# Kernel optimization log

Measured on AMD Instinct MI355X. Metric: run time of the kernel, lower is better.

Reference implementation:

```python
import jax, jax.numpy as jnp
import numpy as np

N_NODES = 131072
N_GRAPHS = 4096
D_Z = 512      # backbone_dout
D_X = 256      # node_dim
D_U = 64       # glob_din
D_H = 512      # dhid
D_IN = D_Z + D_X
N_EDGES = 2097152


def setup_inputs() -> dict:
    key = jax.random.key(0)
    ks = jax.random.split(key, 24)
    s = 0.02
    inp = {
        "z": jax.random.normal(ks[0], (N_NODES, D_Z), jnp.float32),
        "u": jax.random.normal(ks[1], (N_GRAPHS, D_U), jnp.float32),
        "x": jax.random.normal(ks[2], (N_NODES, D_X), jnp.float32),
        "prev_h": jax.random.normal(ks[3], (N_NODES, D_H), jnp.float32),
        "edge_index": jax.random.randint(ks[4], (2, N_EDGES), 0, N_NODES, jnp.int64),
        "batch": jnp.sort(jax.random.randint(ks[5], (N_NODES,), 0, N_GRAPHS, jnp.int64)),
        "batch_size": N_GRAPHS,
        # GConvGRU with K=1: each ChebConv is a plain Linear (T_0 term only)
        "Wxz": jax.random.normal(ks[6], (D_IN, D_H), jnp.float32) * s,
        "bxz": jnp.zeros((D_H,), jnp.float32),
        "Whz": jax.random.normal(ks[7], (D_H, D_H), jnp.float32) * s,
        "bhz": jnp.zeros((D_H,), jnp.float32),
        "Wxr": jax.random.normal(ks[8], (D_IN, D_H), jnp.float32) * s,
        "bxr": jnp.zeros((D_H,), jnp.float32),
        "Whr": jax.random.normal(ks[9], (D_H, D_H), jnp.float32) * s,
        "bhr": jnp.zeros((D_H,), jnp.float32),
        "Wxh": jax.random.normal(ks[10], (D_IN, D_H), jnp.float32) * s,
        "bxh": jnp.zeros((D_H,), jnp.float32),
        "Whh": jax.random.normal(ks[11], (D_H, D_H), jnp.float32) * s,
        "bhh": jnp.zeros((D_H,), jnp.float32),
        # GraphAndGlobalFusion.global_proj
        "Wg": jax.random.normal(ks[12], (D_U, D_Z), jnp.float32) * s,
        "bg": jnp.zeros((D_Z,), jnp.float32),
    }
    return inp


def reference(z, u, x, prev_h, Wxz, bxz, Whz, bhz, Wxr, bxr, Whr, bhr,
              Wxh, bxh, Whh, bhh, Wg, bg, edge_index, batch, batch_size):
    # --- GConvGRU (K=1 ChebConv => per-node linear; edge_index unused) ---
    X = jnp.concatenate([z, x], axis=-1)                       # [N, D_IN]
    Z = jax.nn.sigmoid(X @ Wxz + bxz + prev_h @ Whz + bhz)     # update gate
    R = jax.nn.sigmoid(X @ Wxr + bxr + prev_h @ Whr + bhr)     # reset gate
    H_tilde = jnp.tanh(X @ Wxh + bxh + (prev_h * R) @ Whh + bhh)
    H = Z * prev_h + (1.0 - Z) * H_tilde                       # [N, D_H]
    # --- GraphAndGlobalFusion ---
    graph_emb = jax.ops.segment_sum(z, batch, num_segments=batch_size)  # [B, D_Z]
    glob_emb = jax.nn.relu(u @ Wg + bg)                                 # [B, D_Z]
    fused_emb = jnp.concatenate([graph_emb, glob_emb], axis=-1)         # [B, 2*D_Z]
    return fused_emb, H
```

## Files before the change

### kernel.cpp

```cpp
#include <hip/hip_runtime.h>
#include <hip/hip_bf16.h>

#define N_NODES 131072
#define N_GRAPHS 4096
#define D_Z 512
#define D_X 256
#define D_U 64
#define D_H 512
#define D_IN 768
#define KTOT 1280
#define NG1 1024

using bf16   = __bf16;
using bf16x8 = __attribute__((ext_vector_type(8))) __bf16;
using f32x4  = __attribute__((ext_vector_type(4))) float;
using fl4    = __attribute__((ext_vector_type(4))) float;

__device__ __forceinline__ void gload_lds16(const void* g, void* lds) {
    __builtin_amdgcn_global_load_lds(
        (const __attribute__((address_space(1))) unsigned int*)g,
        (__attribute__((address_space(3))) unsigned int*)lds,
        16, 0, 0);
}

__global__ void prep_weights(const float* __restrict__ Wxz, const float* __restrict__ Whz,
                             const float* __restrict__ Wxr, const float* __restrict__ Whr,
                             const float* __restrict__ Wxh, const float* __restrict__ Whh,
                             const float* __restrict__ bxz, const float* __restrict__ bhz,
                             const float* __restrict__ bxr, const float* __restrict__ bhr,
                             const float* __restrict__ bxh, const float* __restrict__ bhh,
                             bf16* __restrict__ WT1, bf16* __restrict__ WT2,
                             float* __restrict__ bias1, float* __restrict__ bias2)
{
    int idx = blockIdx.x * blockDim.x + threadIdx.x;
    if (idx < NG1)
        bias1[idx] = (idx < D_H) ? (bxz[idx] + bhz[idx]) : (bxr[idx - D_H] + bhr[idx - D_H]);
    if (idx < D_H)
        bias2[idx] = bxh[idx] + bhh[idx];

    const int T1 = NG1 * (KTOT / 8);
    if (idx < T1) {
        int n = idx % NG1, kc = idx / NG1, k0 = kc * 8;
        int col = (n < D_H) ? n : n - D_H;
        const float* Wx = (n < D_H) ? Wxz : Wxr;
        const float* Wh = (n < D_H) ? Whz : Whr;
        bf16x8 o;
        #pragma unroll
        for (int i = 0; i < 8; ++i) {
            int k = k0 + i;
            float f = (k < D_IN) ? Wx[(long)k * D_H + col] : Wh[(long)(k - D_IN) * D_H + col];
            o[i] = (bf16)f;
        }
        *(bf16x8*)(WT1 + (long)n * KTOT + k0) = o;
    } else {
        int j = idx - T1;
        int n = j % D_H, kc = j / D_H, k0 = kc * 8;
        bf16x8 o;
        #pragma unroll
        for (int i = 0; i < 8; ++i) {
            int k = k0 + i;
            float f = (k < D_IN) ? Wxh[(long)k * D_H + n] : Whh[(long)(k - D_IN) * D_H + n];
            o[i] = (bf16)f;
        }
        *(bf16x8*)(WT2 + (long)n * KTOT + k0) = o;
    }
}

__global__ void prep_A(const float* __restrict__ z, const float* __restrict__ x,
                       const float* __restrict__ ph, bf16* __restrict__ Abf)
{
    long idx = (long)blockIdx.x * blockDim.x + threadIdx.x;
    long row = idx / 160;
    int  e   = (int)(idx % 160) * 8;
    const float* src;
    if (e < D_Z)        src = z  + row * D_Z + e;
    else if (e < D_IN)  src = x  + row * D_X + (e - D_Z);
    else                src = ph + row * D_H + (e - D_IN);
    fl4 v0 = *(const fl4*)src;
    fl4 v1 = *(const fl4*)(src + 4);
    bf16x8 o;
    o[0]=(bf16)v0[0]; o[1]=(bf16)v0[1]; o[2]=(bf16)v0[2]; o[3]=(bf16)v0[3];
    o[4]=(bf16)v1[0]; o[5]=(bf16)v1[1]; o[6]=(bf16)v1[2]; o[7]=(bf16)v1[3];
    *(bf16x8*)(Abf + row * KTOT + e) = o;
}

template<int NCOLS, int MODE>
__global__ __launch_bounds__(256, 4)
void gemm_kernel(const bf16* __restrict__ A,
                 const bf16* __restrict__ A2,
                 const bf16* __restrict__ W,
                 const float* __restrict__ bias,
                 float* __restrict__ Hout,
                 bf16* __restrict__ Rapp_out)
{
    __shared__ __align__(16) char Atile[16384];
    __shared__ __align__(16) char Btile[16384];

    const int tid = threadIdx.x;
    const int w = tid >> 6, l = tid & 63;

    constexpr int nb  = NCOLS / 128;
    constexpr int nwg = (N_NODES / 128) * nb;
    constexpr int cpx = nwg / 8;
    const int bid = blockIdx.x;
    const int swz = (bid & 7) * cpx + (bid >> 3);
    const int  bn = swz % nb;
    const long m0 = (long)(swz / nb) * 128;
    const int  n0 = bn * 128;

    const int trow = tid >> 3;
    const int tg   = tid & 7;
    const int kes  = ((tg * 16) ^ ((trow & 7) << 4)) >> 1;

    f32x4 acc[4][4];
    #pragma unroll
    for (int i = 0; i < 4; ++i)
        #pragma unroll
        for (int j = 0; j < 4; ++j) acc[i][j] = f32x4{0.f, 0.f, 0.f, 0.f};

    const int wr = w >> 1, wc = w & 1;
    const int lr = l & 15, lg = l >> 4;

    for (int k0 = 0; k0 < KTOT; k0 += 64) {
        __syncthreads();
        const bf16* Asrc; long astr; int kofs;
        if (MODE == 2 && k0 >= D_IN) { Asrc = A2; astr = D_H;  kofs = k0 - D_IN; }
        else                         { Asrc = A;  astr = KTOT; kofs = k0; }
        #pragma unroll
        for (int r = 0; r < 4; ++r)
            gload_lds16(Asrc + (m0 + r * 32 + trow) * astr + kofs + kes,
                        Atile + r * 4096 + tid * 16);
        #pragma unroll
        for (int r = 0; r < 4; ++r)
            gload_lds16(W + (long)(n0 + r * 32 + trow) * KTOT + k0 + kes,
                        Btile + r * 4096 + tid * 16);
        __syncthreads();

        #pragma unroll
        for (int ks = 0; ks < 2; ++ks) {
            bf16x8 af[4];
            #pragma unroll
            for (int mi = 0; mi < 4; ++mi) {
                int row = wr * 64 + mi * 16 + lr;
                int addr = (row << 7) + ((ks * 64 + lg * 16) ^ ((row & 7) << 4));
                af[mi] = *(const bf16x8*)(Atile + addr);
            }
            #pragma unroll
            for (int ni = 0; ni < 4; ++ni) {
                int row = wc * 64 + ni * 16 + lr;
                int addr = (row << 7) + ((ks * 64 + lg * 16) ^ ((row & 7) << 4));
                bf16x8 bfr = *(const bf16x8*)(Btile + addr);
                #pragma unroll
                for (int mi = 0; mi < 4; ++mi)
                    acc[mi][ni] = __builtin_amdgcn_mfma_f32_16x16x32_bf16(
                        af[mi], bfr, acc[mi][ni], 0, 0, 0);
            }
        }
    }

    #pragma unroll
    for (int mi = 0; mi < 4; ++mi) {
        #pragma unroll
        for (int ni = 0; ni < 4; ++ni) {
            int gc = n0 + wc * 64 + ni * 16 + lr;
            float bv = bias[gc];
            #pragma unroll
            for (int j = 0; j < 4; ++j) {
                long gr = m0 + wr * 64 + mi * 16 + lg * 4 + j;
                float v = acc[mi][ni][j] + bv;
                if (MODE == 1) {
                    float s = 1.f / (1.f + __expf(-v));
                    if (NCOLS == NG1 && n0 < D_H) {
                        Hout[gr * D_H + gc] = s;
                    } else {
                        float ph = (float)A[gr * KTOT + D_IN + (gc - D_H)];
                        Rapp_out[gr * D_H + (gc - D_H)] = (bf16)(s * ph);
                    }
                } else {
                    float ht = 2.f / (1.f + __expf(-2.f * v)) - 1.f;
                    long  o  = gr * D_H + gc;
                    float zz = Hout[o];
                    float ph = (float)A[gr * KTOT + D_IN + gc];
                    Hout[o] = zz * ph + (1.f - zz) * ht;
                }
            }
        }
    }
}

__global__ __launch_bounds__(256)
void fusion_kernel(const float* __restrict__ z, const float* __restrict__ u,
                   const float* __restrict__ Wg, const float* __restrict__ bg,
                   const int* __restrict__ batch, float* __restrict__ out)
{
    int g = blockIdx.x;
    __shared__ float us[D_U];
    __shared__ int   rng[2];
    int tid = threadIdx.x;
    if (tid < D_U) us[tid] = u[(long)g * D_U + tid];
    if (tid < 2) {
        int target = g + tid;
        int lo = 0, hi = N_NODES;
        while (lo < hi) { int mid = (lo + hi) >> 1; if (batch[mid] < target) lo = mid + 1; else hi = mid; }
        rng[tid] = lo;
    }
    __syncthreads();
    int start = rng[0], end = rng[1];
    int d0 = tid * 2;
    float s0 = 0.f, s1 = 0.f;
    for (int n = start; n < end; ++n) {
        const float* zp = z + (long)n * D_Z + d0;
        s0 += zp[0]; s1 += zp[1];
    }
    long ob = (long)g * 1024;
    out[ob + d0]     = s0;
    out[ob + d0 + 1] = s1;
    float a0 = bg[d0], a1 = bg[d0 + 1];
    #pragma unroll 8
    for (int k = 0; k < D_U; ++k) {
        float uv = us[k];
        a0 += uv * Wg[k * D_Z + d0];
        a1 += uv * Wg[k * D_Z + d0 + 1];
    }
    out[ob + 512 + d0]     = fmaxf(a0, 0.f);
    out[ob + 512 + d0 + 1] = fmaxf(a1, 0.f);
}

extern "C" void kernel_launch(void* const* d_in, const int* in_sizes, int n_in,
                              void* d_out, int out_size, void* d_ws, size_t ws_size,
                              hipStream_t stream) {
    (void)in_sizes; (void)n_in; (void)out_size; (void)ws_size;
    const float* z      = (const float*)d_in[0];
    const float* u      = (const float*)d_in[1];
    const float* x      = (const float*)d_in[2];
    const float* prev_h = (const float*)d_in[3];
    const int*   batch  = (const int*)d_in[5];
    const float* Wxz = (const float*)d_in[7];
    const float* bxz = (const float*)d_in[8];
    const float* Whz = (const float*)d_in[9];
    const float* bhz = (const float*)d_in[10];
    const float* Wxr = (const float*)d_in[11];
    const float* bxr = (const float*)d_in[12];
    const float* Whr = (const float*)d_in[13];
    const float* bhr = (const float*)d_in[14];
    const float* Wxh = (const float*)d_in[15];
    const float* bxh = (const float*)d_in[16];
    const float* Whh = (const float*)d_in[17];
    const float* bhh = (const float*)d_in[18];
    const float* Wg  = (const float*)d_in[19];
    const float* bg  = (const float*)d_in[20];

    char* ws = (char*)d_ws;
    bf16*  WT1   = (bf16*)ws;
    bf16*  WT2   = (bf16*)(ws + 2621440);
    float* bias1 = (float*)(ws + 3932160);
    float* bias2 = (float*)(ws + 3936256);
    bf16*  Rapp  = (bf16*)(ws + 4194304);
    bf16*  Abf   = (bf16*)(ws + 4194304 + 134217728);

    float* outF = (float*)d_out;
    float* Hout = outF + (long)N_GRAPHS * 1024;

    hipLaunchKernelGGL(prep_weights, dim3(960), dim3(256), 0, stream,
                       Wxz, Whz, Wxr, Whr, Wxh, Whh,
                       bxz, bhz, bxr, bhr, bxh, bhh,
                       WT1, WT2, bias1, bias2);
    hipLaunchKernelGGL(prep_A, dim3(81920), dim3(256), 0, stream, z, x, prev_h, Abf);
    hipLaunchKernelGGL((gemm_kernel<NG1, 1>), dim3(8192), dim3(256), 0, stream,
                       Abf, (const bf16*)nullptr, WT1, bias1, Hout, Rapp);
    hipLaunchKernelGGL((gemm_kernel<D_H, 2>), dim3(4096), dim3(256), 0, stream,
                       Abf, Rapp, WT2, bias2, Hout, (bf16*)nullptr);
    hipLaunchKernelGGL(fusion_kernel, dim3(N_GRAPHS), dim3(256), 0, stream,
                       z, u, Wg, bg, batch, outF);
}
```

Baseline: 1.082 ms.

## Triple-buffer GEMM LDS tiles with K=32 stages and async prefetch

Replaces the single-buffered K=64 load-then-compute loop with a three-stage LDS ring of K=32 tiles. Global-to-LDS loads are issued two stages ahead, and vmcnt waits plus one barrier per step let the next tiles load while MFMAs run on the current one. The swizzle is changed to fit 64-byte rows. The trade-off is twice as many barriers per K, a shorter MFMA burst per stage, and more LDS per block (48KB vs 32KB), which may reduce occupancy at 4 blocks/CU.

Result: slower. 1.296 ms (+19.8%).

```diff
diff --git a/kernel.cpp b/kernel.cpp
--- a/kernel.cpp
+++ b/kernel.cpp
@@ -93,8 +93,8 @@
                  float* __restrict__ Hout,
                  bf16* __restrict__ Rapp_out)
 {
-    __shared__ __align__(16) char Atile[16384];
-    __shared__ __align__(16) char Btile[16384];
+    __shared__ __align__(16) char Atile[3][8192];
+    __shared__ __align__(16) char Btile[3][8192];
 
     const int tid = threadIdx.x;
     const int w = tid >> 6, l = tid & 63;
@@ -108,9 +108,26 @@
     const long m0 = (long)(swz / nb) * 128;
     const int  n0 = bn * 128;
 
-    const int trow = tid >> 3;
-    const int tg   = tid & 7;
-    const int kes  = ((tg * 16) ^ ((trow & 7) << 4)) >> 1;
+    const int trow = tid >> 2;
+    const int tg   = tid & 3;
+    const int kes  = ((tg * 16) ^ (((trow >> 1) & 3) << 4)) >> 1;
+
+    constexpr int NT = KTOT / 32;
+
+    auto stage = [&](int t, int b) {
+        const int k0 = t * 32;
+        const bf16* Asrc; long astr; int kofs;
+        if (MODE == 2 && k0 >= D_IN) { Asrc = A2; astr = D_H;  kofs = k0 - D_IN; }
+        else                         { Asrc = A;  astr = KTOT; kofs = k0; }
+        #pragma unroll
+        for (int r = 0; r < 2; ++r)
+            gload_lds16(Asrc + (m0 + r * 64 + trow) * astr + kofs + kes,
+                        Atile[b] + r * 4096 + tid * 16);
+        #pragma unroll
+        for (int r = 0; r < 2; ++r)
+            gload_lds16(W + (long)(n0 + r * 64 + trow) * KTOT + k0 + kes,
+                        Btile[b] + r * 4096 + tid * 16);
+    };
 
     f32x4 acc[4][4];
     #pragma unroll
@@ -121,40 +138,38 @@
     const int wr = w >> 1, wc = w & 1;
     const int lr = l & 15, lg = l >> 4;
 
-    for (int k0 = 0; k0 < KTOT; k0 += 64) {
-        __syncthreads();
-        const bf16* Asrc; long astr; int kofs;
-        if (MODE == 2 && k0 >= D_IN) { Asrc = A2; astr = D_H;  kofs = k0 - D_IN; }
-        else                         { Asrc = A;  astr = KTOT; kofs = k0; }
-        #pragma unroll
-        for (int r = 0; r < 4; ++r)
-            gload_lds16(Asrc + (m0 + r * 32 + trow) * astr + kofs + kes,
-                        Atile + r * 4096 + tid * 16);
-        #pragma unroll
-        for (int r = 0; r < 4; ++r)
-            gload_lds16(W + (long)(n0 + r * 32 + trow) * KTOT + k0 + kes,
-                        Btile + r * 4096 + tid * 16);
-        __syncthreads();
-
-        #pragma unroll
-        for (int ks = 0; ks < 2; ++ks) {
-            bf16x8 af[4];
+    auto ldsFrag = [&](const char* base, int row) -> bf16x8 {
+        int byte = (row << 6) + ((lg * 16) ^ (((row >> 1) & 3) << 4));
+        return *(const bf16x8*)(base + byte);
+    };
+
+    stage(0, 0);
+    stage(1, 1);
+    asm volatile("s_waitcnt vmcnt(4)" ::: "memory");
+    __builtin_amdgcn_s_barrier();
+
+    #pragma unroll 1
+    for (int t = 0; t < NT; ++t) {
+        const int cur = t % 3;
+        if (t + 2 < NT) stage(t + 2, (t + 2) % 3);
+
+        bf16x8 af[4];
+        #pragma unroll
+        for (int mi = 0; mi < 4; ++mi)
+            af[mi] = ldsFrag(Atile[cur], wr * 64 + mi * 16 + lr);
+        #pragma unroll
+        for (int ni = 0; ni < 4; ++ni) {
+            bf16x8 bfr = ldsFrag(Btile[cur], wc * 64 + ni * 16 + lr);
             #pragma unroll
-            for (int mi = 0; mi < 4; ++mi) {
-                int row = wr * 64 + mi * 16 + lr;
-                int addr = (row << 7) + ((ks * 64 + lg * 16) ^ ((row & 7) << 4));
-                af[mi] = *(const bf16x8*)(Atile + addr);
-            }
-            #pragma unroll
-            for (int ni = 0; ni < 4; ++ni) {
-                int row = wc * 64 + ni * 16 + lr;
-                int addr = (row << 7) + ((ks * 64 + lg * 16) ^ ((row & 7) << 4));
-                bf16x8 bfr = *(const bf16x8*)(Btile + addr);
-                #pragma unroll
-                for (int mi = 0; mi < 4; ++mi)
-                    acc[mi][ni] = __builtin_amdgcn_mfma_f32_16x16x32_bf16(
-                        af[mi], bfr, acc[mi][ni], 0, 0, 0);
-            }
+            for (int mi = 0; mi < 4; ++mi)
+                acc[mi][ni] = __builtin_amdgcn_mfma_f32_16x16x32_bf16(
+                    af[mi], bfr, acc[mi][ni], 0, 0, 0);
+        }
+
+        if (t + 1 < NT) {
+            if (t + 2 < NT) asm volatile("s_waitcnt vmcnt(4)" ::: "memory");
+            else            asm volatile("s_waitcnt vmcnt(0)" ::: "memory");
+            __builtin_amdgcn_s_barrier();
         }
     }
 
```
